# Performance work log

Hardware: AMD Instinct MI355X
Metric: run time of the kernel (lower is better)

## Reference

```python
import jax, jax.numpy as jnp
import numpy as np

K_LEN, I_LEN, DIM = 1024, 8192, 128


def setup_inputs() -> dict:
    key = jax.random.key(0)
    k1, k2 = jax.random.split(key)
    kernel = jax.random.normal(k1, (K_LEN, DIM), dtype=jnp.float32)
    x = jax.random.normal(k2, (I_LEN, DIM), dtype=jnp.float32)
    return {"kernel": kernel, "x": x}


def _cost_matrix(kernel, x):
    # squared Euclidean pairwise distances, (K, I), via GEMM form
    k2 = jnp.sum(kernel * kernel, axis=-1)  # (K,)
    x2 = jnp.sum(x * x, axis=-1)            # (I,)
    c = k2[:, None] + x2[None, :] - 2.0 * (kernel @ x.T)
    return jnp.maximum(c, 0.0)


def _acc_matrix(c):
    # DTW DP: D[i,j] = c[i,j] + min(D[i-1,j-1], D[i-1,j], D[i,j-1])
    # Row recurrence solved per-row with a (min,+) prefix scan:
    #   e[j] = min(D_prev[j-1], D_prev[j]) + c[j]   (e[0] = D_prev[0] + c[0])
    #   D[j] = S[j] + cummin(e - S),  S = cumsum(c_row)
    row0 = jnp.cumsum(c[0])

    def step(prev, c_row):
        m = jnp.concatenate([prev[:1], jnp.minimum(prev[:-1], prev[1:])])
        e = m + c_row
        S = jnp.cumsum(c_row)
        row = S + jax.lax.cummin(e - S)
        return row, row

    _, rows = jax.lax.scan(step, row0, c[1:])
    return jnp.concatenate([row0[None, :], rows], axis=0)  # (K, I)


def _backtrack(D):
    # tslearn-style backtracking from (K-1, I-1) to (0, 0).
    # Candidate order [diag, up, left]; argmin ties pick first (diag),
    # matching numpy.argmin used by tslearn. Out-of-range -> +inf border.
    K, I = D.shape
    Dp = jnp.full((K + 1, I + 1), jnp.inf, dtype=D.dtype).at[1:, 1:].set(D)
    L = K + I - 1  # max possible path length

    def step(carry, _):
        k, i, fin = carry
        emit = (k, i, jnp.logical_not(fin))
        fin2 = fin | ((k == 0) & (i == 0))
        cand = jnp.stack([Dp[k, i], Dp[k, i + 1], Dp[k + 1, i]])
        a = jnp.argmin(cand)
        nk = jnp.where(fin2, k, k - (a != 2).astype(k.dtype))
        ni = jnp.where(fin2, i, i - (a != 1).astype(i.dtype))
        return (nk, ni, fin2), emit

    init = (jnp.int32(K - 1), jnp.int32(I - 1), jnp.bool_(False))
    _, (ks, iss, valid) = jax.lax.scan(step, init, None, length=L)
    return ks, iss, valid


def reference(kernel, x):
    # Path search uses detached tensors in the original module.
    c = jax.lax.stop_gradient(_cost_matrix(kernel, x))
    D = _acc_matrix(c)
    ks, iss, valid = _backtrack(D)
    # sum of squared diffs along the optimal alignment path (gather + reduce)
    d2 = jnp.sum((kernel[ks] - x[iss]) ** 2, axis=-1)  # (L,)
    return jnp.sum(jnp.where(valid, d2, 0.0))
```

## Files before the change

kernel.cpp:

```cpp
#include <hip/hip_runtime.h>
#include <hip/hip_bf16.h>

typedef unsigned short ushort_t;
typedef unsigned int uint_t;

#define KL 1024
#define IL 8192
#define DIMV 128
#define NS 16
#define NB 258
#define NIT2 270
#define SSH (8256*64)
#define GATE 672
#define INF __builtin_inff()

typedef __attribute__((ext_vector_type(8))) short v8s;
typedef __attribute__((ext_vector_type(4))) float v4f;

__global__ __launch_bounds__(256) void knorms(
    const float* __restrict__ kern, const float* __restrict__ xx,
    float* __restrict__ x2, float* __restrict__ k2, int* __restrict__ flags) {
  if (blockIdx.x == 0 && threadIdx.x < NS) flags[threadIdx.x] = 0;
  const int lane = threadIdx.x & 63;
  const int row = blockIdx.x * 4 + (threadIdx.x >> 6);
  const float* src;
  float* dst;
  if (row < IL) { src = xx + (size_t)row * DIMV; dst = x2 + row; }
  else          { src = kern + (size_t)(row - IL) * DIMV; dst = k2 + (row - IL); }
  float2 v = *(const float2*)(src + lane * 2);
  float ss = v.x * v.x + v.y * v.y;
  #pragma unroll
  for (int off = 32; off > 0; off >>= 1) ss += __shfl_down(ss, off, 64);
  if (lane == 0) *dst = ss;
}

__device__ __forceinline__ v8s pack_bf16x8(float4 a, float4 b) {
  union { unsigned int u[4]; v8s v; } r;
  union { __hip_bfloat162 h; unsigned int u; } t;
  t.h = __float22bfloat162_rn(make_float2(a.x, a.y)); r.u[0] = t.u;
  t.h = __float22bfloat162_rn(make_float2(a.z, a.w)); r.u[1] = t.u;
  t.h = __float22bfloat162_rn(make_float2(b.x, b.y)); r.u[2] = t.u;
  t.h = __float22bfloat162_rn(make_float2(b.z, b.w)); r.u[3] = t.u;
  return r.v;
}

__global__ __launch_bounds__(256) void kgemm(
    const float* __restrict__ kern, const float* __restrict__ xx,
    const float* __restrict__ x2, const float* __restrict__ k2,
    ushort_t* __restrict__ c_h) {
  __shared__ float ctile[64 * 64];
  const int T = threadIdx.x;
  const int w = T >> 6;
  const int lane = T & 63;
  const int lo = lane & 15;
  const int hi = lane >> 4;
  const int i0 = blockIdx.x * 64;
  const int s  = blockIdx.y;
  const int kr0 = s * 64;

  v4f acc[4] = {};
  #pragma unroll
  for (int ks = 0; ks < 4; ks++) {
    const int k = ks * 32 + hi * 8;
    const float* bp = xx + (size_t)(i0 + w * 16 + lo) * DIMV + k;
    v8s bf = pack_bf16x8(*(const float4*)bp, *(const float4*)(bp + 4));
    #pragma unroll
    for (int rt = 0; rt < 4; rt++) {
      const float* ap = kern + (size_t)(kr0 + rt * 16 + lo) * DIMV + k;
      v8s af = pack_bf16x8(*(const float4*)ap, *(const float4*)(ap + 4));
      acc[rt] = __builtin_amdgcn_mfma_f32_16x16x32_bf16(af, bf, acc[rt], 0, 0, 0);
    }
  }
  const float x2v = x2[i0 + w * 16 + lo];
  const int n_local = w * 16 + lo;
  #pragma unroll
  for (int rt = 0; rt < 4; rt++) {
    float4 k2f = *(const float4*)&k2[kr0 + rt * 16 + hi * 4];
    #pragma unroll
    for (int q = 0; q < 4; q++) {
      const int m_local = rt * 16 + hi * 4 + q;
      float cval = fmaxf((&k2f.x)[q] + x2v - 2.f * acc[rt][q], 0.f);
      ctile[n_local * 64 + ((m_local + 2 * n_local) & 63)] = cval;
    }
  }
  __syncthreads();
  _Float16* ob = (_Float16*)(c_h + (size_t)s * SSH);
  #pragma unroll
  for (int q = 0; q < 32; q++) {
    int tt = w + q * 4;
    int di = tt - lane;
    if (tt <= 126 && di >= 0 && di < 64) {
      int t = i0 + tt;
      int tp = t >> 1;
      ob[(((size_t)(tp >> 4) * 1024) + lane * 16 + (tp & 15)) * 2 + (t & 1)] =
          (_Float16)ctile[di * 64 + ((lane + 2 * di) & 63)];
    }
  }
}

__device__ __forceinline__ float dpp_wave_shr1(float oldv, float src) {
  return __int_as_float(__builtin_amdgcn_update_dpp(
      __float_as_int(oldv), __float_as_int(src), 0x138, 0xF, 0xF, false));
}

__global__ __launch_bounds__(320) void kdp(
    const ushort_t* __restrict__ c_h, float* __restrict__ bound,
    int* __restrict__ flags, float* __restrict__ out) {
  __shared__ __align__(16) float ring[4 * 4 * 32];
  __shared__ __align__(16) float feed[4 * 32];
  const int g = blockIdx.x;
  const int wv = threadIdx.x >> 6;
  const int lane = threadIdx.x & 63;
  const int sb = g * 4;

  float Dcur = INF, Dul = INF;
  int fchk = 0, fpend = 0;
  float rfeed = INF;
  const float* bin = bound + (size_t)(sb > 0 ? sb - 1 : 0) * IL;
  float* bout3 = bound + (size_t)(sb + 3) * IL;

  const uint_t* cbase = (const uint_t*)c_h +
      (size_t)(sb + (wv < 4 ? wv : 0)) * (SSH / 2) + lane * 16;

  uint_t P[16], Q[16];

  if (wv < 4) {
    const uint4* sp = (const uint4*)cbase;
    *(uint4*)&P[0] = sp[0]; *(uint4*)&P[4] = sp[1];
    *(uint4*)&P[8] = sp[2]; *(uint4*)&P[12] = sp[3];
    if (g == 0 && wv == 0 && lane == 0) Dcur = 0.f;
  } else {
    if (g > 0) {
      int f;
      do { f = __hip_atomic_load(&flags[sb - 1], __ATOMIC_RELAXED, __HIP_MEMORY_SCOPE_AGENT); } while (f < GATE);
      fchk = f; fpend = f;
      if (lane < 32) {
        feed[lane]      = __hip_atomic_load(&bin[lane],      __ATOMIC_RELAXED, __HIP_MEMORY_SCOPE_AGENT);
        feed[32 + lane] = __hip_atomic_load(&bin[32 + lane], __ATOMIC_RELAXED, __HIP_MEMORY_SCOPE_AGENT);
        rfeed           = __hip_atomic_load(&bin[64 + lane], __ATOMIC_RELAXED, __HIP_MEMORY_SCOPE_AGENT);
      }
    } else {
      if (lane < 32) { feed[lane] = INF; feed[32+lane] = INF; feed[64+lane] = INF; feed[96+lane] = INF; }
    }
  }
  __syncthreads();

  auto body = [&](int i, uint_t (&cur)[16], uint_t (&nxt)[16]) {
    if (wv < 4) {
      const int W = i - 3 * wv;
      int Wn = W + 1; Wn = Wn < 0 ? 0 : (Wn > NB - 1 ? NB - 1 : Wn);
      {
        const uint4* sp = (const uint4*)(cbase + (size_t)Wn * 1024);
        *(uint4*)&nxt[0]  = sp[0]; *(uint4*)&nxt[4]  = sp[1];
        *(uint4*)&nxt[8]  = sp[2]; *(uint4*)&nxt[12] = sp[3];
      }
      if (W >= 0 && W < NB) {
        const float* fb = (wv == 0) ? &feed[(W & 3) * 32]
                                    : &ring[(wv - 1) * 128 + (W & 3) * 32];
        float fv[32];
        #pragma unroll
        for (int q = 0; q < 8; q++) {
          float4 f4 = *(const float4*)(fb + q * 4);
          fv[4 * q]     = f4.x; fv[4 * q + 1] = f4.y;
          fv[4 * q + 2] = f4.z; fv[4 * q + 3] = f4.w;
        }
        float cvv[32];
        #pragma unroll
        for (int tp = 0; tp < 16; tp++) {
          union { uint_t u; _Float16 h[2]; } cu; cu.u = cur[tp];
          cvv[2 * tp]     = (float)cu.h[0];
          cvv[2 * tp + 1] = (float)cu.h[1];
        }
        float bb[32];
        if (W >= 2 && W < 256) {
          #pragma unroll
          for (int tt = 0; tt < 32; tt++) {
            float Dup = dpp_wave_shr1(fv[tt], Dcur);
            float m1 = fminf(Dul, Dcur);
            Dcur = cvv[tt] + fminf(m1, Dup);
            Dul = Dup;
            bb[tt] = Dcur;
          }
        } else {
          const int t0 = W * 32;
          #pragma unroll
          for (int tt = 0; tt < 32; tt++) {
            const int t = t0 + tt;
            float Dup = dpp_wave_shr1(fv[tt], Dcur);
            float m1 = fminf(Dul, Dcur);
            float Dnew = cvv[tt] + fminf(m1, Dup);
            const bool alo = (t >= lane);
            const bool ahi = (t - lane < IL);
            if (alo) Dul = Dup;
            if (alo && ahi) Dcur = Dnew;
            bb[tt] = Dcur;
          }
        }
        if (lane == 63) {
          const int base2 = wv * 128 + (((W - 2) & 3) << 5);
          const int base1 = wv * 128 + (((W - 1) & 3) << 5);
          if (W >= 2) {
            #pragma unroll
            for (int tt = 0; tt < 31; tt++) ring[base2 + tt + 1] = bb[tt];
          }
          if (W >= 1) ring[base1] = bb[31];
        }
      }
      asm volatile("s_waitcnt lgkmcnt(0)" ::: "memory");
      __builtin_amdgcn_s_barrier();
    } else {
      asm volatile("s_waitcnt vmcnt(0)" ::: "memory");
      if (g > 0) {
        if (fpend > fchk) fchk = fpend;
        const int Fw = i + 2;
        if (Fw >= 2 && Fw <= 255 && lane < 32) feed[(Fw & 3) * 32 + lane] = rfeed;
        const int Fl = i + 3;
        if (Fl <= 255) {
          const int need = 32 * (Fl + 1);
          if (fchk < need) {
            int f;
            do { f = __hip_atomic_load(&flags[sb - 1], __ATOMIC_RELAXED, __HIP_MEMORY_SCOPE_AGENT); } while (f < need);
            fchk = f;
          }
          if (lane < 32)
            rfeed = __hip_atomic_load(&bin[32 * Fl + lane], __ATOMIC_RELAXED, __HIP_MEMORY_SCOPE_AGENT);
        }
        fpend = __hip_atomic_load(&flags[sb - 1], __ATOMIC_RELAXED, __HIP_MEMORY_SCOPE_AGENT);
      }
      if (g < 3) {
        const int E = i - 12;
        if (E >= 0 && E < 256 && lane < 32) {
          float bv2 = ring[3 * 128 + (E & 3) * 32 + lane];
          __hip_atomic_store(&bout3[32 * E + lane], bv2, __ATOMIC_RELAXED, __HIP_MEMORY_SCOPE_AGENT);
        }
        const int Ep = i - 13;
        if (Ep >= 0 && Ep < 256 && lane == 0)
          __hip_atomic_store(&flags[sb + 3], 32 * Ep + 32, __ATOMIC_RELAXED, __HIP_MEMORY_SCOPE_AGENT);
      }
      asm volatile("s_waitcnt lgkmcnt(0)" ::: "memory");
      __builtin_amdgcn_s_barrier();
    }
  };

  for (int i = 0; i < NIT2; i += 2) {
    body(i, P, Q);
    body(i + 1, Q, P);
  }

  asm volatile("s_waitcnt vmcnt(0)" ::: "memory");
  if (g == 3 && wv == 3 && lane == 63) out[0] = Dcur;
}

extern "C" void kernel_launch(void* const* d_in, const int* in_sizes, int n_in,
                              void* d_out, int out_size, void* d_ws, size_t ws_size,
                              hipStream_t stream) {
  const float* kern = (const float*)d_in[0];
  const float* xx   = (const float*)d_in[1];
  char* ws = (char*)d_ws;
  const size_t OFF_X2 = (size_t)NS * SSH * 2;
  const size_t OFF_K2 = OFF_X2 + (size_t)IL * 4;
  const size_t OFF_BD = OFF_K2 + (size_t)KL * 4;
  const size_t OFF_FL = OFF_BD + (size_t)NS * IL * 4;
  ushort_t* c_h  = (ushort_t*)ws;
  float* x2    = (float*)(ws + OFF_X2);
  float* k2    = (float*)(ws + OFF_K2);
  float* bnd   = (float*)(ws + OFF_BD);
  int*   flags = (int*)(ws + OFF_FL);

  knorms<<<(IL + KL) / 4, 256, 0, stream>>>(kern, xx, x2, k2, flags);
  kgemm<<<dim3(IL / 64, NS), 256, 0, stream>>>(kern, xx, x2, k2, c_h);
  kdp<<<4, 320, 0, stream>>>(c_h, bnd, flags, (float*)d_out);
}
```

Before: 466.5 us.

## Merge four chained DP blocks into one 16-wave block with LDS handoff

The DTW wavefront moves from four cooperating blocks into a single 1024-thread block. Before, the blocks exchanged boundary rows through global memory, with atomic flags, a feeder wave per block and spin-waits. Now all 16 waves in one workgroup pass boundary rows through a shared-memory ring, with a barrier per step and an iteration count sized for the 16-wave skew. This removes the cross-block global-memory latency and the gate delays, but puts four waves on each SIMD of a single CU, so the latency-bound scan chains now compete for issue slots.

Result: slower. 600.7 us (+28.8%).

```diff
diff --git a/kernel.cpp b/kernel.cpp
--- a/kernel.cpp
+++ b/kernel.cpp
@@ -9,9 +9,8 @@
 #define DIMV 128
 #define NS 16
 #define NB 258
-#define NIT2 270
+#define NIT2 304
 #define SSH (8256*64)
-#define GATE 672
 #define INF __builtin_inff()
 
 typedef __attribute__((ext_vector_type(8))) short v8s;
@@ -19,8 +18,7 @@
 
 __global__ __launch_bounds__(256) void knorms(
     const float* __restrict__ kern, const float* __restrict__ xx,
-    float* __restrict__ x2, float* __restrict__ k2, int* __restrict__ flags) {
-  if (blockIdx.x == 0 && threadIdx.x < NS) flags[threadIdx.x] = 0;
+    float* __restrict__ x2, float* __restrict__ k2) {
   const int lane = threadIdx.x & 63;
   const int row = blockIdx.x * 4 + (threadIdx.x >> 6);
   const float* src;
@@ -103,143 +101,92 @@
       __float_as_int(oldv), __float_as_int(src), 0x138, 0xF, 0xF, false));
 }
 
-__global__ __launch_bounds__(320) void kdp(
-    const ushort_t* __restrict__ c_h, float* __restrict__ bound,
-    int* __restrict__ flags, float* __restrict__ out) {
-  __shared__ __align__(16) float ring[4 * 4 * 32];
-  __shared__ __align__(16) float feed[4 * 32];
-  const int g = blockIdx.x;
+__global__ __launch_bounds__(1024, 4) void kdp(
+    const ushort_t* __restrict__ c_h, float* __restrict__ out) {
+  __shared__ __align__(16) float ring[16 * 4 * 32];
   const int wv = threadIdx.x >> 6;
   const int lane = threadIdx.x & 63;
-  const int sb = g * 4;
 
   float Dcur = INF, Dul = INF;
-  int fchk = 0, fpend = 0;
-  float rfeed = INF;
-  const float* bin = bound + (size_t)(sb > 0 ? sb - 1 : 0) * IL;
-  float* bout3 = bound + (size_t)(sb + 3) * IL;
-
-  const uint_t* cbase = (const uint_t*)c_h +
-      (size_t)(sb + (wv < 4 ? wv : 0)) * (SSH / 2) + lane * 16;
+  if (wv == 0 && lane == 0) Dcur = 0.f;
+
+  const uint_t* cbase = (const uint_t*)c_h + (size_t)wv * (SSH / 2) + lane * 16;
 
   uint_t P[16], Q[16];
 
-  if (wv < 4) {
+  {
     const uint4* sp = (const uint4*)cbase;
     *(uint4*)&P[0] = sp[0]; *(uint4*)&P[4] = sp[1];
     *(uint4*)&P[8] = sp[2]; *(uint4*)&P[12] = sp[3];
-    if (g == 0 && wv == 0 && lane == 0) Dcur = 0.f;
-  } else {
-    if (g > 0) {
-      int f;
-      do { f = __hip_atomic_load(&flags[sb - 1], __ATOMIC_RELAXED, __HIP_MEMORY_SCOPE_AGENT); } while (f < GATE);
-      fchk = f; fpend = f;
-      if (lane < 32) {
-        feed[lane]      = __hip_atomic_load(&bin[lane],      __ATOMIC_RELAXED, __HIP_MEMORY_SCOPE_AGENT);
-        feed[32 + lane] = __hip_atomic_load(&bin[32 + lane], __ATOMIC_RELAXED, __HIP_MEMORY_SCOPE_AGENT);
-        rfeed           = __hip_atomic_load(&bin[64 + lane], __ATOMIC_RELAXED, __HIP_MEMORY_SCOPE_AGENT);
-      }
-    } else {
-      if (lane < 32) { feed[lane] = INF; feed[32+lane] = INF; feed[64+lane] = INF; feed[96+lane] = INF; }
-    }
   }
   __syncthreads();
 
   auto body = [&](int i, uint_t (&cur)[16], uint_t (&nxt)[16]) {
-    if (wv < 4) {
-      const int W = i - 3 * wv;
-      int Wn = W + 1; Wn = Wn < 0 ? 0 : (Wn > NB - 1 ? NB - 1 : Wn);
-      {
-        const uint4* sp = (const uint4*)(cbase + (size_t)Wn * 1024);
-        *(uint4*)&nxt[0]  = sp[0]; *(uint4*)&nxt[4]  = sp[1];
-        *(uint4*)&nxt[8]  = sp[2]; *(uint4*)&nxt[12] = sp[3];
-      }
-      if (W >= 0 && W < NB) {
-        const float* fb = (wv == 0) ? &feed[(W & 3) * 32]
-                                    : &ring[(wv - 1) * 128 + (W & 3) * 32];
-        float fv[32];
+    const int W = i - 3 * wv;
+    int Wn = W + 1; Wn = Wn < 0 ? 0 : (Wn > NB - 1 ? NB - 1 : Wn);
+    {
+      const uint4* sp = (const uint4*)(cbase + (size_t)Wn * 1024);
+      *(uint4*)&nxt[0]  = sp[0]; *(uint4*)&nxt[4]  = sp[1];
+      *(uint4*)&nxt[8]  = sp[2]; *(uint4*)&nxt[12] = sp[3];
+    }
+    if (W >= 0 && W < NB) {
+      float fv[32];
+      if (wv == 0) {
+        #pragma unroll
+        for (int tt = 0; tt < 32; tt++) fv[tt] = INF;
+      } else {
+        const float* fb = &ring[(wv - 1) * 128 + (W & 3) * 32];
         #pragma unroll
         for (int q = 0; q < 8; q++) {
           float4 f4 = *(const float4*)(fb + q * 4);
           fv[4 * q]     = f4.x; fv[4 * q + 1] = f4.y;
           fv[4 * q + 2] = f4.z; fv[4 * q + 3] = f4.w;
         }
-        float cvv[32];
-        #pragma unroll
-        for (int tp = 0; tp < 16; tp++) {
-          union { uint_t u; _Float16 h[2]; } cu; cu.u = cur[tp];
-          cvv[2 * tp]     = (float)cu.h[0];
-          cvv[2 * tp + 1] = (float)cu.h[1];
-        }
-        float bb[32];
-        if (W >= 2 && W < 256) {
+      }
+      float cvv[32];
+      #pragma unroll
+      for (int tp = 0; tp < 16; tp++) {
+        union { uint_t u; _Float16 h[2]; } cu; cu.u = cur[tp];
+        cvv[2 * tp]     = (float)cu.h[0];
+        cvv[2 * tp + 1] = (float)cu.h[1];
+      }
+      float bb[32];
+      if (W >= 2 && W < 256) {
+        #pragma unroll
+        for (int tt = 0; tt < 32; tt++) {
+          float Dup = dpp_wave_shr1(fv[tt], Dcur);
+          float m1 = fminf(Dul, Dcur);
+          Dcur = cvv[tt] + fminf(m1, Dup);
+          Dul = Dup;
+          bb[tt] = Dcur;
+        }
+      } else {
+        const int t0 = W * 32;
+        #pragma unroll
+        for (int tt = 0; tt < 32; tt++) {
+          const int t = t0 + tt;
+          float Dup = dpp_wave_shr1(fv[tt], Dcur);
+          float m1 = fminf(Dul, Dcur);
+          float Dnew = cvv[tt] + fminf(m1, Dup);
+          const bool alo = (t >= lane);
+          const bool ahi = (t - lane < IL);
+          if (alo) Dul = Dup;
+          if (alo && ahi) Dcur = Dnew;
+          bb[tt] = Dcur;
+        }
+      }
+      if (lane == 63) {
+        const int base2 = wv * 128 + (((W - 2) & 3) << 5);
+        const int base1 = wv * 128 + (((W - 1) & 3) << 5);
+        if (W >= 2) {
           #pragma unroll
-          for (int tt = 0; tt < 32; tt++) {
-            float Dup = dpp_wave_shr1(fv[tt], Dcur);
-            float m1 = fminf(Dul, Dcur);
-            Dcur = cvv[tt] + fminf(m1, Dup);
-            Dul = Dup;
-            bb[tt] = Dcur;
-          }
-        } else {
-          const int t0 = W * 32;
-          #pragma unroll
-          for (int tt = 0; tt < 32; tt++) {
-            const int t = t0 + tt;
-            float Dup = dpp_wave_shr1(fv[tt], Dcur);
-            float m1 = fminf(Dul, Dcur);
-            float Dnew = cvv[tt] + fminf(m1, Dup);
-            const bool alo = (t >= lane);
-            const bool ahi = (t - lane < IL);
-            if (alo) Dul = Dup;
-            if (alo && ahi) Dcur = Dnew;
-            bb[tt] = Dcur;
-          }
-        }
-        if (lane == 63) {
-          const int base2 = wv * 128 + (((W - 2) & 3) << 5);
-          const int base1 = wv * 128 + (((W - 1) & 3) << 5);
-          if (W >= 2) {
-            #pragma unroll
-            for (int tt = 0; tt < 31; tt++) ring[base2 + tt + 1] = bb[tt];
-          }
-          if (W >= 1) ring[base1] = bb[31];
-        }
-      }
-      asm volatile("s_waitcnt lgkmcnt(0)" ::: "memory");
-      __builtin_amdgcn_s_barrier();
-    } else {
-      asm volatile("s_waitcnt vmcnt(0)" ::: "memory");
-      if (g > 0) {
-        if (fpend > fchk) fchk = fpend;
-        const int Fw = i + 2;
-        if (Fw >= 2 && Fw <= 255 && lane < 32) feed[(Fw & 3) * 32 + lane] = rfeed;
-        const int Fl = i + 3;
-        if (Fl <= 255) {
-          const int need = 32 * (Fl + 1);
-          if (fchk < need) {
-            int f;
-            do { f = __hip_atomic_load(&flags[sb - 1], __ATOMIC_RELAXED, __HIP_MEMORY_SCOPE_AGENT); } while (f < need);
-            fchk = f;
-          }
-          if (lane < 32)
-            rfeed = __hip_atomic_load(&bin[32 * Fl + lane], __ATOMIC_RELAXED, __HIP_MEMORY_SCOPE_AGENT);
-        }
-        fpend = __hip_atomic_load(&flags[sb - 1], __ATOMIC_RELAXED, __HIP_MEMORY_SCOPE_AGENT);
-      }
-      if (g < 3) {
-        const int E = i - 12;
-        if (E >= 0 && E < 256 && lane < 32) {
-          float bv2 = ring[3 * 128 + (E & 3) * 32 + lane];
-          __hip_atomic_store(&bout3[32 * E + lane], bv2, __ATOMIC_RELAXED, __HIP_MEMORY_SCOPE_AGENT);
-        }
-        const int Ep = i - 13;
-        if (Ep >= 0 && Ep < 256 && lane == 0)
-          __hip_atomic_store(&flags[sb + 3], 32 * Ep + 32, __ATOMIC_RELAXED, __HIP_MEMORY_SCOPE_AGENT);
-      }
-      asm volatile("s_waitcnt lgkmcnt(0)" ::: "memory");
-      __builtin_amdgcn_s_barrier();
-    }
+          for (int tt = 0; tt < 31; tt++) ring[base2 + tt + 1] = bb[tt];
+        }
+        if (W >= 1) ring[base1] = bb[31];
+      }
+    }
+    asm volatile("s_waitcnt lgkmcnt(0)" ::: "memory");
+    __builtin_amdgcn_s_barrier();
   };
 
   for (int i = 0; i < NIT2; i += 2) {
@@ -248,7 +195,7 @@
   }
 
   asm volatile("s_waitcnt vmcnt(0)" ::: "memory");
-  if (g == 3 && wv == 3 && lane == 63) out[0] = Dcur;
+  if (wv == 15 && lane == 63) out[0] = Dcur;
 }
 
 extern "C" void kernel_launch(void* const* d_in, const int* in_sizes, int n_in,
@@ -259,15 +206,11 @@
   char* ws = (char*)d_ws;
   const size_t OFF_X2 = (size_t)NS * SSH * 2;
   const size_t OFF_K2 = OFF_X2 + (size_t)IL * 4;
-  const size_t OFF_BD = OFF_K2 + (size_t)KL * 4;
-  const size_t OFF_FL = OFF_BD + (size_t)NS * IL * 4;
   ushort_t* c_h  = (ushort_t*)ws;
   float* x2    = (float*)(ws + OFF_X2);
   float* k2    = (float*)(ws + OFF_K2);
-  float* bnd   = (float*)(ws + OFF_BD);
-  int*   flags = (int*)(ws + OFF_FL);
-
-  knorms<<<(IL + KL) / 4, 256, 0, stream>>>(kern, xx, x2, k2, flags);
+
+  knorms<<<(IL + KL) / 4, 256, 0, stream>>>(kern, xx, x2, k2);
   kgemm<<<dim3(IL / 64, NS), 256, 0, stream>>>(kern, xx, x2, k2, c_h);
-  kdp<<<4, 320, 0, stream>>>(c_h, bnd, flags, (float*)d_out);
-}
+  kdp<<<1, 1024, 0, stream>>>(c_h, (float*)d_out);
+}
```
